# Performance work log

Hardware: AMD Instinct MI355X
Metric: run time of the kernel (lower is better)

Reference implementation:

```python
import jax, jax.numpy as jnp
import numpy as np

B, T, D, H = 8192, 128, 16, 32
EPS = 1e-5  # BatchNorm1d default eps (eval mode, running stats)


def setup_inputs() -> dict:
    key = jax.random.key(0)
    ks = iter(jax.random.split(key, 64))

    def nrm(shape, s=0.1):
        return jax.random.normal(next(ks), shape, jnp.float32) * s

    inp = {}
    inp["S"] = nrm((B, T, D), 1.0)
    inp["g_S"] = nrm((B, T), 1.0)
    inp["times"] = jnp.linspace(0.0, 1.0, T, dtype=jnp.float32)
    inp["payoff_T"] = nrm((B,), 1.0)
    inp["delta_T"] = nrm((B, D), 1.0)
    # init_hidden: uniform(-0.1, 0.1), shape [num_layers=2, B, H]
    inp["h_price0"] = jax.random.uniform(next(ks), (2, B, H), jnp.float32, -0.1, 0.1)
    inp["h_delta0"] = jax.random.uniform(next(ks), (2, B, H), jnp.float32, -0.1, 0.1)
    # params for price net (prefix p_, out_dim=1) and delta net (prefix d_, out_dim=D)
    for pfx, out_dim in (("p", 1), ("d", D)):
        inp[pfx + "_Wih0"] = nrm((3 * H, 2 * D))
        inp[pfx + "_Whh0"] = nrm((3 * H, H))
        inp[pfx + "_bih0"] = nrm((3 * H,))
        inp[pfx + "_bhh0"] = nrm((3 * H,))
        inp[pfx + "_Wih1"] = nrm((3 * H, H))
        inp[pfx + "_Whh1"] = nrm((3 * H, H))
        inp[pfx + "_bih1"] = nrm((3 * H,))
        inp[pfx + "_bhh1"] = nrm((3 * H,))
        inp[pfx + "_embW"] = nrm((H, H))
        inp[pfx + "_embB"] = nrm((H,))
        inp[pfx + "_bng"] = jnp.ones((H,), jnp.float32)
        inp[pfx + "_bnb"] = jnp.zeros((H,), jnp.float32)
        inp[pfx + "_bnm"] = nrm((H,))
        inp[pfx + "_bnv"] = jax.random.uniform(next(ks), (H,), jnp.float32, 0.5, 1.5)
        inp[pfx + "_outW"] = nrm((out_dim, H))
        inp[pfx + "_outB"] = nrm((out_dim,))
    return inp


def _gru_cell(x, h, Wih, Whh, bih, bhh):
    # PyTorch GRU cell, gate order (r, z, n)
    gi = x @ Wih.T + bih
    gh = h @ Whh.T + bhh
    ir, iz, inn = jnp.split(gi, 3, axis=-1)
    hr, hz, hn = jnp.split(gh, 3, axis=-1)
    r = jax.nn.sigmoid(ir + hr)
    z = jax.nn.sigmoid(iz + hz)
    n = jnp.tanh(inn + r * hn)
    return (1.0 - z) * n + z * h


def _head(y, Wemb, bemb, g, b, m, v, Wout, bout, sig):
    # Linear -> BatchNorm1d (eval, running stats) -> SiLU -> Linear [-> Sigmoid]
    e = y @ Wemb.T + bemb
    e = (e - m) * jax.lax.rsqrt(v + EPS) * g + b
    e = e * jax.nn.sigmoid(e)  # SiLU
    o = e @ Wout.T + bout
    return jax.nn.sigmoid(o) if sig else o


def reference(S, g_S, times, payoff_T, delta_T, h_price0, h_delta0,
              p_Wih0, p_Whh0, p_bih0, p_bhh0, p_Wih1, p_Whh1, p_bih1, p_bhh1,
              p_embW, p_embB, p_bng, p_bnb, p_bnm, p_bnv, p_outW, p_outB,
              d_Wih0, d_Whh0, d_bih0, d_bhh0, d_Wih1, d_Whh1, d_bih1, d_bhh1,
              d_embW, d_embB, d_bng, d_bnb, d_bnm, d_bnv, d_outW, d_outB):
    # X = cat([S, g_S expanded to d]) -> [B, T, 2D]
    gS = jnp.broadcast_to(g_S[..., None], S.shape)
    X = jnp.concatenate([S, gS], axis=-1)
    Xr = jnp.swapaxes(X, 0, 1)[::-1]  # [T, B, 2D], time reversed (loop goes t=T-1..0)

    def step(carry, xt):
        hp0, hp1, hd0, hd1 = carry
        hp0 = _gru_cell(xt, hp0, p_Wih0, p_Whh0, p_bih0, p_bhh0)
        hp1 = _gru_cell(hp0, hp1, p_Wih1, p_Whh1, p_bih1, p_bhh1)
        hd0 = _gru_cell(xt, hd0, d_Wih0, d_Whh0, d_bih0, d_bhh0)
        hd1 = _gru_cell(hd0, hd1, d_Wih1, d_Whh1, d_bih1, d_bhh1)
        return (hp0, hp1, hd0, hd1), (hp1, hd1)

    carry0 = (h_price0[0], h_price0[1], h_delta0[0], h_delta0[1])
    _, (Yp, Yd) = jax.lax.scan(step, carry0, Xr)
    # flip time back to forward order: outputs were collected for t=T-1..0
    Yp = jnp.swapaxes(Yp[::-1], 0, 1)  # [B, T, H]
    Yd = jnp.swapaxes(Yd[::-1], 0, 1)  # [B, T, H]
    prices = _head(Yp, p_embW, p_embB, p_bng, p_bnb, p_bnm, p_bnv, p_outW, p_outB, False)  # [B,T,1]
    deltas = _head(Yd, d_embW, d_embB, d_bng, d_bnb, d_bnm, d_bnv, d_outW, d_outB, True)   # [B,T,D]
    return (prices, deltas)
```

## Files before the change

kernel.cpp:

```cpp
#include <hip/hip_runtime.h>
#include <hip/hip_bf16.h>
#include <stdint.h>

#define DI __device__ __forceinline__

typedef float f32x4 __attribute__((ext_vector_type(4)));
typedef short bf16x8 __attribute__((ext_vector_type(8)));

constexpr int BB = 8192, TT = 128, DD = 16, HH = 32;
constexpr float kEPS = 1e-5f;
constexpr float kLOG2E = 1.44269504088896340736f;

DI float rcpf_(float x) { return __builtin_amdgcn_rcpf(x); }
DI float exp2f_(float x) { return __builtin_amdgcn_exp2f(x); }
DI float sigm(float x) { return rcpf_(1.0f + exp2f_(-kLOG2E * x)); }

DI uint32_t cvtpk(float lo, float hi) {
  uint32_t r;
  asm("v_cvt_pk_bf16_f32 %0, %1, %2" : "=v"(r) : "v"(lo), "v"(hi));
  return r;
}

DI f32x4 mfma_(bf16x8 a, bf16x8 b, f32x4 c) {
  return __builtin_amdgcn_mfma_f32_16x16x32_bf16(a, b, c, 0, 0, 0);
}

#define PIN(x) asm volatile("" : "+v"(x))

union U4 { uint4 q; bf16x8 v; };

__global__ void prep_net(const float* Wih0, const float* Whh0,
                         const float* bih0, const float* bhh0,
                         const float* Wih1, const float* Whh1,
                         const float* bih1, const float* bhh1,
                         const float* embW, const float* embB,
                         const float* bng, const float* bnb,
                         const float* bnm, const float* bnv,
                         const float* outW, const float* outB,
                         int outDim, uint8_t* wsbase) {
  int tid = threadIdx.x;
  uint16_t* W = (uint16_t*)wsbase;
  float* bias = (float*)(wsbase + 27648);
  auto cvt = [](float f) -> uint16_t {
    union { float f; uint32_t u; } v; v.f = f;
    uint32_t u = v.u;
    return (uint16_t)((u + 0x7FFF + ((u >> 16) & 1)) >> 16);
  };
  for (int idx = tid; idx < 27 * 64; idx += 256) {
    int tile = idx >> 6, l = idx & 63, cc = l & 15, gg = l >> 4;
    uint16_t* dst = W + (size_t)idx * 8;
    if (tile < 24) {
      const float* mats[4] = {Wih0, Whh0, Wih1, Whh1};
      const float* src = mats[tile / 6];
      int sub = tile % 6;
      int row = sub * 16 + cc;
      float sc = (sub < 4) ? -kLOG2E : 2.0f * kLOG2E;
#pragma unroll
      for (int j = 0; j < 8; ++j) dst[j] = cvt(src[row * 32 + 8 * gg + j] * sc);
    } else if (tile < 26) {
      int row = (tile - 24) * 16 + cc;
      float a = bng[row] * rsqrtf(bnv[row] + kEPS);
#pragma unroll
      for (int j = 0; j < 8; ++j) dst[j] = cvt(embW[row * 32 + 8 * gg + j] * a);
    } else {
      int rrow = (cc < outDim) ? cc : 0;
      float sc = (cc < outDim) ? 1.0f : 0.0f;
#pragma unroll
      for (int j = 0; j < 8; ++j) dst[j] = cvt(outW[rrow * 32 + 8 * gg + j] * sc);
    }
  }
  for (int idx = tid; idx < 304; idx += 256) {
    int tile = idx >> 4, n = idx & 15;
    float v;
    if (tile < 8) {
      if (tile < 4)      v = (bih0[tile * 16 + n] + bhh0[tile * 16 + n]) * (-kLOG2E);
      else if (tile < 6) v = bih0[64 + (tile - 4) * 16 + n] * (2.0f * kLOG2E);
      else               v = bhh0[64 + (tile - 6) * 16 + n] * (2.0f * kLOG2E);
    } else if (tile < 16) {
      int tt = tile - 8;
      if (tt < 4)        v = (bih1[tt * 16 + n] + bhh1[tt * 16 + n]) * (-kLOG2E);
      else if (tt < 6)   v = bih1[64 + (tt - 4) * 16 + n] * (2.0f * kLOG2E);
      else               v = bhh1[64 + (tt - 6) * 16 + n] * (2.0f * kLOG2E);
    } else if (tile < 18) {
      int nn = (tile - 16) * 16 + n;
      float a = bng[nn] * rsqrtf(bnv[nn] + kEPS);
      v = a * (embB[nn] - bnm[nn]) + bnb[nn];
    } else {
      v = (n < outDim) ? outB[n] : 0.0f;
    }
    bias[idx] = v;
  }
}

__global__ __launch_bounds__(128, 2) void rnn_fused(
    const float* __restrict__ S, const float* __restrict__ gS,
    const float* __restrict__ hp0, const float* __restrict__ hd0,
    const uint8_t* __restrict__ ws, float* __restrict__ out) {
  const int tid = threadIdx.x, lane = tid & 63, wid = tid >> 6;
  const int net = blockIdx.x & 1;
  const int b0 = (blockIdx.x >> 1) * 16;
  const int c = lane & 15, g = lane >> 4;

  const uint16_t* W = (const uint16_t*)(ws + net * 32768);
  const float* bias = (const float*)(ws + net * 32768 + 27648);
  const float* hsrc = net ? hd0 : hp0;

  __shared__ uint4 ring0[8][64];
  __shared__ volatile int flags[2];
  if (tid < 2) flags[tid] = 0;
  __syncthreads();

  auto waitGE = [&](int idx, int target) {
    if (flags[idx] >= target) return;
    do { __builtin_amdgcn_s_sleep(1); } while (flags[idx] < target);
  };

  const int addr0 = ((lane & 15) | ((lane & 16) << 1)) << 2;
  const int addr1 = addr0 + 64;
  const bool lo32 = lane < 32;
  auto regroup = [&](const float (&v)[8]) -> bf16x8 {
    int P0 = (int)cvtpk(v[0], v[1]), P1 = (int)cvtpk(v[2], v[3]);
    int Q0 = (int)cvtpk(v[4], v[5]), Q1 = (int)cvtpk(v[6], v[7]);
    union { uint32_t u[4]; bf16x8 r; } t;
    int a, b;
    a = __builtin_amdgcn_ds_bpermute(addr0, P0);
    b = __builtin_amdgcn_ds_bpermute(addr0, Q0);
    t.u[0] = lo32 ? a : b;
    a = __builtin_amdgcn_ds_bpermute(addr0, P1);
    b = __builtin_amdgcn_ds_bpermute(addr0, Q1);
    t.u[1] = lo32 ? a : b;
    a = __builtin_amdgcn_ds_bpermute(addr1, P0);
    b = __builtin_amdgcn_ds_bpermute(addr1, Q0);
    t.u[2] = lo32 ? a : b;
    a = __builtin_amdgcn_ds_bpermute(addr1, P1);
    b = __builtin_amdgcn_ds_bpermute(addr1, Q1);
    t.u[3] = lo32 ? a : b;
    return t.r;
  };

  auto gruStep = [&](const bf16x8 (&Wi)[6], const bf16x8 (&Wh)[6],
                     const f32x4 (&Bb)[8], bf16x8 xf, bf16x8 hf,
                     float (&hC)[8]) {
    f32x4 r0 = mfma_(Wi[0], xf, Bb[0]); r0 = mfma_(Wh[0], hf, r0);
    f32x4 r1 = mfma_(Wi[1], xf, Bb[1]); r1 = mfma_(Wh[1], hf, r1);
    f32x4 z0 = mfma_(Wi[2], xf, Bb[2]); z0 = mfma_(Wh[2], hf, z0);
    f32x4 z1 = mfma_(Wi[3], xf, Bb[3]); z1 = mfma_(Wh[3], hf, z1);
    f32x4 ni0 = mfma_(Wi[4], xf, Bb[4]);
    f32x4 ni1 = mfma_(Wi[5], xf, Bb[5]);
    f32x4 nh0 = mfma_(Wh[4], hf, Bb[6]);
    f32x4 nh1 = mfma_(Wh[5], hf, Bb[7]);
#pragma unroll
    for (int r = 0; r < 4; ++r) {
      float rg0 = rcpf_(1.0f + exp2f_(r0[r]));
      float rg1 = rcpf_(1.0f + exp2f_(r1[r]));
      float w0 = ni0[r] + rg0 * nh0[r];
      float w1 = ni1[r] + rg1 * nh1[r];
      float En0 = exp2f_(w0), En1 = exp2f_(w1);
      float Ez0 = exp2f_(z0[r]), Ez1 = exp2f_(z1[r]);
      float hv0 = hC[r], hv1 = hC[4 + r];
      float num0 = (hv0 - Ez0) + En0 * (hv0 + Ez0);
      float num1 = (hv1 - Ez1) + En1 * (hv1 + Ez1);
      float den0 = (1.0f + En0) * (1.0f + Ez0);
      float den1 = (1.0f + En1) * (1.0f + Ez1);
      hC[r]     = num0 * rcpf_(den0);
      hC[4 + r] = num1 * rcpf_(den1);
    }
  };

  auto mkB = [&](const float* row) -> bf16x8 {
    f32x4 a = *(const f32x4*)(row);
    f32x4 b = *(const f32x4*)(row + 4);
    union { uint32_t u[4]; bf16x8 v; } t;
    t.u[0] = cvtpk(a[0], a[1]); t.u[1] = cvtpk(a[2], a[3]);
    t.u[2] = cvtpk(b[0], b[1]); t.u[3] = cvtpk(b[2], b[3]);
    return t.v;
  };

  if (wid == 0) {
    bf16x8 Wi[6], Wh[6];
#pragma unroll
    for (int t = 0; t < 6; ++t) {
      Wi[t] = *(const bf16x8*)(W + ((0 + t) * 64 + lane) * 8);
      Wh[t] = *(const bf16x8*)(W + ((6 + t) * 64 + lane) * 8);
      PIN(Wi[t]); PIN(Wh[t]);
    }
    f32x4 Bb[8];
#pragma unroll
    for (int t = 0; t < 8; ++t) {
      Bb[t] = *(const f32x4*)(bias + t * 16 + 4 * g);
      PIN(Bb[t]);
    }

    float h0C[8];
#pragma unroll
    for (int r = 0; r < 4; ++r) {
      h0C[r]     = hsrc[(size_t)(b0 + c) * HH + 4 * g + r];
      h0C[4 + r] = hsrc[(size_t)(b0 + c) * HH + 16 + 4 * g + r];
    }
    bf16x8 h0B = mkB(hsrc + (size_t)(b0 + c) * HH + 8 * g);

    auto mkX = [&](f32x4 sa, f32x4 sb, float gsv) -> bf16x8 {
      uint32_t pkg = cvtpk(gsv, gsv);
      union { uint32_t u[4]; bf16x8 v; } t;
      uint32_t p0 = cvtpk(sa[0], sa[1]), p1 = cvtpk(sa[2], sa[3]);
      uint32_t p2 = cvtpk(sb[0], sb[1]), p3 = cvtpk(sb[2], sb[3]);
      t.u[0] = lo32 ? p0 : pkg;
      t.u[1] = lo32 ? p1 : pkg;
      t.u[2] = lo32 ? p2 : pkg;
      t.u[3] = lo32 ? p3 : pkg;
      return t.v;
    };

    const float* Sbase  = S  + (size_t)(b0 + c) * TT * DD + 8 * (g & 1);
    const float* gSbase = gS + (size_t)(b0 + c) * TT;

    f32x4 sa0 = *(const f32x4*)(Sbase + (size_t)(TT - 1) * DD);
    f32x4 sb0 = *(const f32x4*)(Sbase + (size_t)(TT - 1) * DD + 4);
    float gv0 = gSbase[TT - 1];
    f32x4 sa1 = *(const f32x4*)(Sbase + (size_t)(TT - 2) * DD);
    f32x4 sb1 = *(const f32x4*)(Sbase + (size_t)(TT - 2) * DD + 4);
    float gv1 = gSbase[TT - 2];

#pragma unroll 2
    for (int i = 0; i < TT; ++i) {
      int tn = TT - 3 - i; if (tn < 0) tn = 0;
      const float* p = Sbase + (size_t)tn * DD;
      f32x4 san = *(const f32x4*)p, sbn = *(const f32x4*)(p + 4);
      float gvn = gSbase[tn];

      bf16x8 xB = mkX(sa0, sb0, gv0);
      gruStep(Wi, Wh, Bb, xB, h0B, h0C);
      h0B = regroup(h0C);

      if (i >= 7) waitGE(1, i - 7);
      asm volatile("" ::: "memory");
      { U4 u; u.v = h0B; ring0[i & 7][lane] = u.q; }
      asm volatile("s_waitcnt lgkmcnt(0)" ::: "memory");
      if (lane == 0) flags[0] = i + 1;

      sa0 = sa1; sb0 = sb1; gv0 = gv1;
      sa1 = san; sb1 = sbn; gv1 = gvn;
    }
  } else {
    bf16x8 Wi[6], Wh[6], We0, We1, Wo;
#pragma unroll
    for (int t = 0; t < 6; ++t) {
      Wi[t] = *(const bf16x8*)(W + ((12 + t) * 64 + lane) * 8);
      Wh[t] = *(const bf16x8*)(W + ((18 + t) * 64 + lane) * 8);
      PIN(Wi[t]); PIN(Wh[t]);
    }
    We0 = *(const bf16x8*)(W + (24 * 64 + lane) * 8);
    We1 = *(const bf16x8*)(W + (25 * 64 + lane) * 8);
    Wo  = *(const bf16x8*)(W + (26 * 64 + lane) * 8);
    PIN(We0); PIN(We1); PIN(Wo);
    f32x4 Bb[8];
#pragma unroll
    for (int t = 0; t < 8; ++t) {
      Bb[t] = *(const f32x4*)(bias + (8 + t) * 16 + 4 * g);
      PIN(Bb[t]);
    }
    f32x4 Be0 = *(const f32x4*)(bias + 16 * 16 + 4 * g);
    f32x4 Be1 = *(const f32x4*)(bias + 17 * 16 + 4 * g);
    f32x4 Bo  = *(const f32x4*)(bias + 18 * 16 + 4 * g);
    PIN(Be0); PIN(Be1); PIN(Bo);

    float h1C[8];
#pragma unroll
    for (int r = 0; r < 4; ++r) {
      h1C[r]     = hsrc[((size_t)BB + b0 + c) * HH + 4 * g + r];
      h1C[4 + r] = hsrc[((size_t)BB + b0 + c) * HH + 16 + 4 * g + r];
    }
    bf16x8 h1B = mkB(hsrc + ((size_t)BB + b0 + c) * HH + 8 * g);

    auto head = [&](bf16x8 h1f, int th) {
      f32x4 e0 = mfma_(We0, h1f, Be0);
      f32x4 e1 = mfma_(We1, h1f, Be1);
      float es[8];
#pragma unroll
      for (int r = 0; r < 4; ++r) {
        float a = e0[r], b = e1[r];
        es[r]     = a * sigm(a);
        es[4 + r] = b * sigm(b);
      }
      bf16x8 ef = regroup(es);
      f32x4 o = mfma_(Wo, ef, Bo);
      if (net == 0) {
        if (lane < 16) out[(size_t)(b0 + c) * TT + th] = o[0];
      } else {
        f32x4 so;
#pragma unroll
        for (int r = 0; r < 4; ++r) so[r] = sigm(o[r]);
        *(f32x4*)(out + (size_t)BB * TT +
                  ((size_t)(b0 + c) * TT + th) * DD + 4 * g) = so;
      }
    };

#pragma unroll 1
    for (int i = 0; i < TT; ++i) {
      waitGE(0, i + 1);
      asm volatile("" ::: "memory");
      U4 u; u.q = ring0[i & 7][lane];
      asm volatile("s_waitcnt lgkmcnt(0)" ::: "memory");
      if (lane == 0) flags[1] = i + 1;

      bf16x8 h1prev = h1B;
      gruStep(Wi, Wh, Bb, u.v, h1B, h1C);
      if (i > 0) head(h1prev, TT - i);
      h1B = regroup(h1C);
    }
    head(h1B, 0);
  }
}

extern "C" void kernel_launch(void* const* d_in, const int* in_sizes, int n_in,
                              void* d_out, int out_size, void* d_ws,
                              size_t ws_size, hipStream_t stream) {
  const float* S   = (const float*)d_in[0];
  const float* gS  = (const float*)d_in[1];
  const float* hp0 = (const float*)d_in[5];
  const float* hd0 = (const float*)d_in[6];
  uint8_t* ws = (uint8_t*)d_ws;

  prep_net<<<1, 256, 0, stream>>>(
      (const float*)d_in[7],  (const float*)d_in[8],  (const float*)d_in[9],
      (const float*)d_in[10], (const float*)d_in[11], (const float*)d_in[12],
      (const float*)d_in[13], (const float*)d_in[14], (const float*)d_in[15],
      (const float*)d_in[16], (const float*)d_in[17], (const float*)d_in[18],
      (const float*)d_in[19], (const float*)d_in[20], (const float*)d_in[21],
      (const float*)d_in[22], 1, ws);
  prep_net<<<1, 256, 0, stream>>>(
      (const float*)d_in[23], (const float*)d_in[24], (const float*)d_in[25],
      (const float*)d_in[26], (const float*)d_in[27], (const float*)d_in[28],
      (const float*)d_in[29], (const float*)d_in[30], (const float*)d_in[31],
      (const float*)d_in[32], (const float*)d_in[33], (const float*)d_in[34],
      (const float*)d_in[35], (const float*)d_in[36], (const float*)d_in[37],
      (const float*)d_in[38], 16, ws + 32768);

  rnn_fused<<<dim3((BB / 16) * 2), dim3(128), 0, stream>>>(S, gS, hp0, hd0,
                                                           ws, (float*)d_out);
}
```

Measured before the change: 163.5 us.

## Permute weight K-order to drop bpermute regroup and batch ring-buffer flag syncs

The K dimension of the bf16 weight tiles is reordered in the prep kernel so that each lane's MFMA output registers can be packed straight into the B operand of the next step. This replaces the eight ds_bpermute cross-lane shuffles per regroup with plain packing. The input x is loaded with the matching per-lane layout, and the inter-wave handshake between the layer-0 producer and layer-1 consumer now updates and waits on flags once every four steps instead of every step. PIN register constraints are dropped. The coarser synchronization adds latency between the two waves, and it only stays correct if the ring depth and permutation are consistent.

```diff
diff --git a/kernel.cpp b/kernel.cpp
--- a/kernel.cpp
+++ b/kernel.cpp
@@ -25,9 +25,7 @@
   return __builtin_amdgcn_mfma_f32_16x16x32_bf16(a, b, c, 0, 0, 0);
 }
 
-#define PIN(x) asm volatile("" : "+v"(x))
-
-union U4 { uint4 q; bf16x8 v; };
+union U4 { uint4 q; bf16x8 v; uint32_t u[4]; };
 
 __global__ void prep_net(const float* Wih0, const float* Whh0,
                          const float* bih0, const float* bhh0,
@@ -56,17 +54,26 @@
       int row = sub * 16 + cc;
       float sc = (sub < 4) ? -kLOG2E : 2.0f * kLOG2E;
 #pragma unroll
-      for (int j = 0; j < 8; ++j) dst[j] = cvt(src[row * 32 + 8 * gg + j] * sc);
+      for (int j = 0; j < 8; ++j) {
+        int k = (j < 4) ? 4 * gg + j : 16 + 4 * gg + (j - 4);
+        dst[j] = cvt(src[row * 32 + k] * sc);
+      }
     } else if (tile < 26) {
       int row = (tile - 24) * 16 + cc;
       float a = bng[row] * rsqrtf(bnv[row] + kEPS);
 #pragma unroll
-      for (int j = 0; j < 8; ++j) dst[j] = cvt(embW[row * 32 + 8 * gg + j] * a);
+      for (int j = 0; j < 8; ++j) {
+        int k = (j < 4) ? 4 * gg + j : 16 + 4 * gg + (j - 4);
+        dst[j] = cvt(embW[row * 32 + k] * a);
+      }
     } else {
       int rrow = (cc < outDim) ? cc : 0;
       float sc = (cc < outDim) ? 1.0f : 0.0f;
 #pragma unroll
-      for (int j = 0; j < 8; ++j) dst[j] = cvt(outW[rrow * 32 + 8 * gg + j] * sc);
+      for (int j = 0; j < 8; ++j) {
+        int k = (j < 4) ? 4 * gg + j : 16 + 4 * gg + (j - 4);
+        dst[j] = cvt(outW[rrow * 32 + k] * sc);
+      }
     }
   }
   for (int idx = tid; idx < 304; idx += 256) {
@@ -115,27 +122,11 @@
     do { __builtin_amdgcn_s_sleep(1); } while (flags[idx] < target);
   };
 
-  const int addr0 = ((lane & 15) | ((lane & 16) << 1)) << 2;
-  const int addr1 = addr0 + 64;
-  const bool lo32 = lane < 32;
-  auto regroup = [&](const float (&v)[8]) -> bf16x8 {
-    int P0 = (int)cvtpk(v[0], v[1]), P1 = (int)cvtpk(v[2], v[3]);
-    int Q0 = (int)cvtpk(v[4], v[5]), Q1 = (int)cvtpk(v[6], v[7]);
-    union { uint32_t u[4]; bf16x8 r; } t;
-    int a, b;
-    a = __builtin_amdgcn_ds_bpermute(addr0, P0);
-    b = __builtin_amdgcn_ds_bpermute(addr0, Q0);
-    t.u[0] = lo32 ? a : b;
-    a = __builtin_amdgcn_ds_bpermute(addr0, P1);
-    b = __builtin_amdgcn_ds_bpermute(addr0, Q1);
-    t.u[1] = lo32 ? a : b;
-    a = __builtin_amdgcn_ds_bpermute(addr1, P0);
-    b = __builtin_amdgcn_ds_bpermute(addr1, Q0);
-    t.u[2] = lo32 ? a : b;
-    a = __builtin_amdgcn_ds_bpermute(addr1, P1);
-    b = __builtin_amdgcn_ds_bpermute(addr1, Q1);
-    t.u[3] = lo32 ? a : b;
-    return t.r;
+  auto packB = [&](const float (&v)[8]) -> bf16x8 {
+    U4 t;
+    t.u[0] = cvtpk(v[0], v[1]); t.u[1] = cvtpk(v[2], v[3]);
+    t.u[2] = cvtpk(v[4], v[5]); t.u[3] = cvtpk(v[6], v[7]);
+    return t.v;
   };
 
   auto gruStep = [&](const bf16x8 (&Wi)[6], const bf16x8 (&Wh)[6],
@@ -167,10 +158,12 @@
     }
   };
 
-  auto mkB = [&](const float* row) -> bf16x8 {
-    f32x4 a = *(const f32x4*)(row);
-    f32x4 b = *(const f32x4*)(row + 4);
-    union { uint32_t u[4]; bf16x8 v; } t;
+  auto loadState = [&](const float* row, float (&hC)[8]) -> bf16x8 {
+    f32x4 a = *(const f32x4*)(row + 4 * g);
+    f32x4 b = *(const f32x4*)(row + 16 + 4 * g);
+#pragma unroll
+    for (int r = 0; r < 4; ++r) { hC[r] = a[r]; hC[4 + r] = b[r]; }
+    U4 t;
     t.u[0] = cvtpk(a[0], a[1]); t.u[1] = cvtpk(a[2], a[3]);
     t.u[2] = cvtpk(b[0], b[1]); t.u[3] = cvtpk(b[2], b[3]);
     return t.v;
@@ -182,64 +175,53 @@
     for (int t = 0; t < 6; ++t) {
       Wi[t] = *(const bf16x8*)(W + ((0 + t) * 64 + lane) * 8);
       Wh[t] = *(const bf16x8*)(W + ((6 + t) * 64 + lane) * 8);
-      PIN(Wi[t]); PIN(Wh[t]);
     }
     f32x4 Bb[8];
 #pragma unroll
-    for (int t = 0; t < 8; ++t) {
+    for (int t = 0; t < 8; ++t)
       Bb[t] = *(const f32x4*)(bias + t * 16 + 4 * g);
-      PIN(Bb[t]);
-    }
 
     float h0C[8];
-#pragma unroll
-    for (int r = 0; r < 4; ++r) {
-      h0C[r]     = hsrc[(size_t)(b0 + c) * HH + 4 * g + r];
-      h0C[4 + r] = hsrc[(size_t)(b0 + c) * HH + 16 + 4 * g + r];
-    }
-    bf16x8 h0B = mkB(hsrc + (size_t)(b0 + c) * HH + 8 * g);
-
-    auto mkX = [&](f32x4 sa, f32x4 sb, float gsv) -> bf16x8 {
+    bf16x8 h0B = loadState(hsrc + (size_t)(b0 + c) * HH, h0C);
+
+    auto mkX = [&](f32x4 sv, float gsv) -> bf16x8 {
       uint32_t pkg = cvtpk(gsv, gsv);
-      union { uint32_t u[4]; bf16x8 v; } t;
-      uint32_t p0 = cvtpk(sa[0], sa[1]), p1 = cvtpk(sa[2], sa[3]);
-      uint32_t p2 = cvtpk(sb[0], sb[1]), p3 = cvtpk(sb[2], sb[3]);
-      t.u[0] = lo32 ? p0 : pkg;
-      t.u[1] = lo32 ? p1 : pkg;
-      t.u[2] = lo32 ? p2 : pkg;
-      t.u[3] = lo32 ? p3 : pkg;
+      U4 t;
+      t.u[0] = cvtpk(sv[0], sv[1]);
+      t.u[1] = cvtpk(sv[2], sv[3]);
+      t.u[2] = pkg;
+      t.u[3] = pkg;
       return t.v;
     };
 
-    const float* Sbase  = S  + (size_t)(b0 + c) * TT * DD + 8 * (g & 1);
+    const float* Sbase  = S  + (size_t)(b0 + c) * TT * DD + 4 * g;
     const float* gSbase = gS + (size_t)(b0 + c) * TT;
 
-    f32x4 sa0 = *(const f32x4*)(Sbase + (size_t)(TT - 1) * DD);
-    f32x4 sb0 = *(const f32x4*)(Sbase + (size_t)(TT - 1) * DD + 4);
+    f32x4 sv0 = *(const f32x4*)(Sbase + (size_t)(TT - 1) * DD);
     float gv0 = gSbase[TT - 1];
-    f32x4 sa1 = *(const f32x4*)(Sbase + (size_t)(TT - 2) * DD);
-    f32x4 sb1 = *(const f32x4*)(Sbase + (size_t)(TT - 2) * DD + 4);
+    f32x4 sv1 = *(const f32x4*)(Sbase + (size_t)(TT - 2) * DD);
     float gv1 = gSbase[TT - 2];
 
 #pragma unroll 2
     for (int i = 0; i < TT; ++i) {
       int tn = TT - 3 - i; if (tn < 0) tn = 0;
-      const float* p = Sbase + (size_t)tn * DD;
-      f32x4 san = *(const f32x4*)p, sbn = *(const f32x4*)(p + 4);
+      f32x4 svn = *(const f32x4*)(Sbase + (size_t)tn * DD);
       float gvn = gSbase[tn];
 
-      bf16x8 xB = mkX(sa0, sb0, gv0);
+      bf16x8 xB = mkX(sv0, gv0);
       gruStep(Wi, Wh, Bb, xB, h0B, h0C);
-      h0B = regroup(h0C);
-
-      if (i >= 7) waitGE(1, i - 7);
+      h0B = packB(h0C);
+
+      if (i >= 8 && (i & 3) == 0) waitGE(1, i - 4);
       asm volatile("" ::: "memory");
       { U4 u; u.v = h0B; ring0[i & 7][lane] = u.q; }
-      asm volatile("s_waitcnt lgkmcnt(0)" ::: "memory");
-      if (lane == 0) flags[0] = i + 1;
-
-      sa0 = sa1; sb0 = sb1; gv0 = gv1;
-      sa1 = san; sb1 = sbn; gv1 = gvn;
+      if ((i & 3) == 3) {
+        asm volatile("s_waitcnt lgkmcnt(0)" ::: "memory");
+        if (lane == 0) flags[0] = i + 1;
+      }
+
+      sv0 = sv1; gv0 = gv1;
+      sv1 = svn; gv1 = gvn;
     }
   } else {
     bf16x8 Wi[6], Wh[6], We0, We1, Wo;
@@ -247,30 +229,20 @@
     for (int t = 0; t < 6; ++t) {
       Wi[t] = *(const bf16x8*)(W + ((12 + t) * 64 + lane) * 8);
       Wh[t] = *(const bf16x8*)(W + ((18 + t) * 64 + lane) * 8);
-      PIN(Wi[t]); PIN(Wh[t]);
     }
     We0 = *(const bf16x8*)(W + (24 * 64 + lane) * 8);
     We1 = *(const bf16x8*)(W + (25 * 64 + lane) * 8);
     Wo  = *(const bf16x8*)(W + (26 * 64 + lane) * 8);
-    PIN(We0); PIN(We1); PIN(Wo);
     f32x4 Bb[8];
 #pragma unroll
-    for (int t = 0; t < 8; ++t) {
+    for (int t = 0; t < 8; ++t)
       Bb[t] = *(const f32x4*)(bias + (8 + t) * 16 + 4 * g);
-      PIN(Bb[t]);
-    }
-    f32x4 Be0 = *(const f32x4*)(bias + 16 * 16 + 4 * g);
-    f32x4 Be1 = *(const f32x4*)(bias + 17 * 16 + 4 * g);
-    f32x4 Bo  = *(const f32x4*)(bias + 18 * 16 + 4 * g);
-    PIN(Be0); PIN(Be1); PIN(Bo);
+    const f32x4 Be0 = *(const f32x4*)(bias + 16 * 16 + 4 * g);
+    const f32x4 Be1 = *(const f32x4*)(bias + 17 * 16 + 4 * g);
+    const f32x4 Bo  = *(const f32x4*)(bias + 18 * 16 + 4 * g);
 
     float h1C[8];
-#pragma unroll
-    for (int r = 0; r < 4; ++r) {
-      h1C[r]     = hsrc[((size_t)BB + b0 + c) * HH + 4 * g + r];
-      h1C[4 + r] = hsrc[((size_t)BB + b0 + c) * HH + 16 + 4 * g + r];
-    }
-    bf16x8 h1B = mkB(hsrc + ((size_t)BB + b0 + c) * HH + 8 * g);
+    bf16x8 h1B = loadState(hsrc + ((size_t)BB + b0 + c) * HH, h1C);
 
     auto head = [&](bf16x8 h1f, int th) {
       f32x4 e0 = mfma_(We0, h1f, Be0);
@@ -282,7 +254,7 @@
         es[r]     = a * sigm(a);
         es[4 + r] = b * sigm(b);
       }
-      bf16x8 ef = regroup(es);
+      bf16x8 ef = packB(es);
       f32x4 o = mfma_(Wo, ef, Bo);
       if (net == 0) {
         if (lane < 16) out[(size_t)(b0 + c) * TT + th] = o[0];
@@ -297,16 +269,16 @@
 
 #pragma unroll 1
     for (int i = 0; i < TT; ++i) {
-      waitGE(0, i + 1);
+      if ((i & 3) == 0) waitGE(0, i + 4);
       asm volatile("" ::: "memory");
       U4 u; u.q = ring0[i & 7][lane];
       asm volatile("s_waitcnt lgkmcnt(0)" ::: "memory");
-      if (lane == 0) flags[1] = i + 1;
+      if ((i & 3) == 3 && lane == 0) flags[1] = i + 1;
 
       bf16x8 h1prev = h1B;
       gruStep(Wi, Wh, Bb, u.v, h1B, h1C);
       if (i > 0) head(h1prev, TT - i);
-      h1B = regroup(h1C);
+      h1B = packB(h1C);
     }
     head(h1B, 0);
   }
```

New measurement: 151.4 us. 1.08x faster.
